# Performance work log

Measured on AMD Instinct MI355X. Metric: run time of the kernel, lower is better.

Reference implementation:

```python
import jax, jax.numpy as jnp
import numpy as np

LEAKY_SLOPE = 0.2  # LeakyReLU(0.2) attention activation from the torch module
HEADS = 4
RATES = (10, 25)


def _prod(v):
    r = 1
    for x in v:
        r *= x
    return r


def gat_conv(x_self, x_neigh, W, a_s, a_n):
    """Single GAT aggregation layer (aggregate_method='concat').
    x_self:  [..., F_in]
    x_neigh: [..., E, F_in] (leading dims reshape-compatible with x_self)
    W: [F_in, H*D], a_s/a_n: [H, D]
    Returns [..., H*D].
    """
    H = HEADS
    D = W.shape[1] // H
    lead = x_self.shape[:-1]
    E = x_neigh.shape[-2]
    z_s = (x_self @ W).reshape(lead + (H, D))                  # [..., H, D]
    z_n = (x_neigh @ W).reshape(lead + (E, H, D))              # [..., E, H, D]
    e_s = jnp.einsum('...hd,hd->...h', z_s, a_s)               # [..., H]
    e_n = jnp.einsum('...ehd,hd->...eh', z_n, a_n)             # [..., E, H]
    logits = jax.nn.leaky_relu(e_s[..., None, :] + e_n, LEAKY_SLOPE)
    alpha = jax.nn.softmax(logits, axis=-2)                    # softmax over neighbors E
    out = jnp.einsum('...eh,...ehd->...hd', alpha, z_n)        # attention-weighted sum
    return out.reshape(lead + (H * D,))


def setup_inputs() -> dict:
    key = jax.random.key(0)
    ks = jax.random.split(key, 10)
    B, F, HID, OUT = 1024, 128, 512, 256
    s = 0.05
    return {
        'h0': jax.random.normal(ks[0], (B, F), jnp.float32),
        'h1': jax.random.normal(ks[1], (B, RATES[0], F), jnp.float32),
        'h2': jax.random.normal(ks[2], (B, RATES[0] * RATES[1], F), jnp.float32),
        'W0': jax.random.normal(ks[3], (F, HID), jnp.float32) * s,
        'a0_s': jax.random.normal(ks[4], (HEADS, HID // HEADS), jnp.float32) * s,
        'a0_n': jax.random.normal(ks[5], (HEADS, HID // HEADS), jnp.float32) * s,
        'W1': jax.random.normal(ks[6], (HID, HID), jnp.float32) * s,
        'a1_s': jax.random.normal(ks[7], (HEADS, HID // HEADS), jnp.float32) * s,
        'a1_n': jax.random.normal(ks[8], (HEADS, HID // HEADS), jnp.float32) * s,
        'W_fc': jax.random.normal(ks[9], (HID, OUT), jnp.float32) * s,
    }


def reference(h0, h1, h2, W0, a0_s, a0_n, W1, a1_s, a1_n, W_fc):
    B = h0.shape[0]
    hs = [h0, h1, h2]
    layers = [(W0, a0_s, a0_n), (W1, a1_s, a1_n)]
    depth = len(RATES)
    # hierarchical sweep: layer i is applied to levels 0..depth-i-1
    for i, (W, a_s, a_n) in enumerate(layers):
        for j in range(depth - i):
            x_self = hs[j]
            x_neigh = hs[j + 1].reshape(B, _prod(RATES[:j]), RATES[j], -1)
            hs[j] = gat_conv(x_self, x_neigh, W, a_s, a_n)
    return hs[0] @ W_fc  # final Linear (no bias, no activation)
```

## Files before the change

### kernel.cpp

```cpp
#include <hip/hip_runtime.h>

__device__ __forceinline__ void gemm32(
    float* __restrict__ smem,
    const float* __restrict__ A, int lda,
    const float* __restrict__ B, int ldb,
    float* __restrict__ C, int ldc, int K,
    int m0, int col0) {
  float* As = smem;
  float* Bs = smem + 16 * 36;
  const int t = threadIdx.x;
  const int tn = t & 31, tm = t >> 5;
  const int lam = t >> 2, lak = (t & 3) * 4;
  const int lbk = t >> 4, lbn = (t & 15) * 8;
  float acc[4][4];
#pragma unroll
  for (int i = 0; i < 4; ++i)
#pragma unroll
    for (int j = 0; j < 4; ++j) acc[i][j] = 0.f;
  for (int k0 = 0; k0 < K; k0 += 16) {
    if (t < 128) {
      float4 av = *reinterpret_cast<const float4*>(A + (size_t)(m0 + lam) * lda + k0 + lak);
      As[(lak + 0) * 36 + lam] = av.x;
      As[(lak + 1) * 36 + lam] = av.y;
      As[(lak + 2) * 36 + lam] = av.z;
      As[(lak + 3) * 36 + lam] = av.w;
    }
    const float* bp = B + (size_t)(k0 + lbk) * ldb + col0 + lbn;
    float4 b0 = *reinterpret_cast<const float4*>(bp);
    float4 b1 = *reinterpret_cast<const float4*>(bp + 4);
    float* bd = &Bs[lbk * 132 + lbn];
    *reinterpret_cast<float4*>(bd) = b0;
    *reinterpret_cast<float4*>(bd + 4) = b1;
    __syncthreads();
#pragma unroll
    for (int kk = 0; kk < 16; ++kk) {
      float4 a4 = *reinterpret_cast<const float4*>(&As[kk * 36 + tm * 4]);
      float4 b4 = *reinterpret_cast<const float4*>(&Bs[kk * 132 + tn * 4]);
      float a[4] = {a4.x, a4.y, a4.z, a4.w};
      float b[4] = {b4.x, b4.y, b4.z, b4.w};
#pragma unroll
      for (int i = 0; i < 4; ++i)
#pragma unroll
        for (int j = 0; j < 4; ++j) acc[i][j] = fmaf(a[i], b[j], acc[i][j]);
    }
    __syncthreads();
  }
#pragma unroll
  for (int i = 0; i < 4; ++i) {
    float* cp = C + (size_t)(m0 + tm * 4 + i) * ldc + col0 + tn * 4;
    *reinterpret_cast<float4*>(cp) =
        make_float4(acc[i][0], acc[i][1], acc[i][2], acc[i][3]);
  }
}

template <int E>
__device__ __forceinline__ void gat128_item(
    float* __restrict__ smem,
    const float* __restrict__ xs, const float* __restrict__ xn,
    const float* __restrict__ waS, const float* __restrict__ waN,
    float* __restrict__ outp) {
  constexpr int MR = E + 1;
  constexpr int PASSES = (MR + 7) / 8;
  float* tile = smem;
  float* partial = smem + E * 128;
  const int t = threadIdx.x;
  const int el = t >> 5;
  const int f0 = (t & 31) * 4;
  float4 pre[PASSES];
#pragma unroll
  for (int p = 0; p < PASSES; ++p) {
    int e = p * 8 + el;
    if (e < E) pre[p] = *reinterpret_cast<const float4*>(xn + (size_t)e * 128 + f0);
    else if (e == E) pre[p] = *reinterpret_cast<const float4*>(xs + f0);
  }
  float4 wn[4], ws[4];
#pragma unroll
  for (int h = 0; h < 4; ++h) {
    wn[h] = *reinterpret_cast<const float4*>(waN + h * 128 + f0);
    ws[h] = *reinterpret_cast<const float4*>(waS + h * 128 + f0);
  }
#pragma unroll
  for (int p = 0; p < PASSES; ++p) {
    int e = p * 8 + el;
    if (e < MR) {
      float4 x = pre[p];
      if (e < E) *reinterpret_cast<float4*>(tile + e * 128 + f0) = x;
      float ph[4];
#pragma unroll
      for (int h = 0; h < 4; ++h) {
        float4 w = (e < E) ? wn[h] : ws[h];
        ph[h] = x.x * w.x + x.y * w.y + x.z * w.z + x.w * w.w;
      }
      const int b0 = t & 1, b1 = (t >> 1) & 1;
      float m0 = b0 ? ph[1] : ph[0];
      float o0 = b0 ? ph[0] : ph[1];
      float m1 = b0 ? ph[3] : ph[2];
      float o1 = b0 ? ph[2] : ph[3];
      m0 += __shfl_xor(o0, 1);
      m1 += __shfl_xor(o1, 1);
      float mk = b1 ? m1 : m0;
      float gv = b1 ? m0 : m1;
      mk += __shfl_xor(gv, 2);
      mk += __shfl_xor(mk, 4);
      mk += __shfl_xor(mk, 8);
      mk += __shfl_xor(mk, 16);
      if ((t & 31) < 4) partial[e * 4 + (t & 3)] = mk;
    }
  }
  __syncthreads();
  const int w = t >> 6, l = t & 63;
  float selfl = partial[E * 4 + w];
  float xv = -1e30f;
  if (l < E) {
    float x = selfl + partial[l * 4 + w];
    xv = (x > 0.f) ? x : 0.2f * x;
  }
  float m = xv;
  m = fmaxf(m, __shfl_xor(m, 1));
  m = fmaxf(m, __shfl_xor(m, 2));
  m = fmaxf(m, __shfl_xor(m, 4));
  m = fmaxf(m, __shfl_xor(m, 8));
  m = fmaxf(m, __shfl_xor(m, 16));
  m = fmaxf(m, __shfl_xor(m, 32));
  float pz = (l < E) ? __expf(xv - m) : 0.f;
  float s = pz;
  s += __shfl_xor(s, 1);
  s += __shfl_xor(s, 2);
  s += __shfl_xor(s, 4);
  s += __shfl_xor(s, 8);
  s += __shfl_xor(s, 16);
  s += __shfl_xor(s, 32);
  float alpha = pz * (1.f / s);
  float2 acc = make_float2(0.f, 0.f);
#pragma unroll
  for (int e = 0; e < E; ++e) {
    float a = __shfl(alpha, e);
    float2 x = *reinterpret_cast<const float2*>(tile + e * 128 + l * 2);
    acc.x = fmaf(a, x.x, acc.x);
    acc.y = fmaf(a, x.y, acc.y);
  }
  *reinterpret_cast<float2*>(outp + w * 128 + l * 2) = acc;
}

__device__ __forceinline__ void gat512_item(
    float* __restrict__ tile, float* __restrict__ partial,
    const float* __restrict__ xs, const float* __restrict__ xn,
    const float* __restrict__ vaS, const float* __restrict__ vaN,
    float* __restrict__ outp) {
  const int t = threadIdx.x;
  const int el = t >> 7, f0 = (t & 127) * 4;
  float4 vn[4], vs[4];
#pragma unroll
  for (int h = 0; h < 4; ++h) {
    vn[h] = *reinterpret_cast<const float4*>(vaN + h * 512 + f0);
    vs[h] = *reinterpret_cast<const float4*>(vaS + h * 512 + f0);
  }
#pragma unroll
  for (int p = 0; p < 6; ++p) {
    int e = p * 2 + el;
    if (e < 11) {
      const float* src = (e < 10) ? (xn + (size_t)e * 512 + f0) : (xs + f0);
      float4 x = *reinterpret_cast<const float4*>(src);
      if (e < 10) *reinterpret_cast<float4*>(tile + e * 512 + f0) = x;
      float ph[4];
#pragma unroll
      for (int h = 0; h < 4; ++h) {
        float4 w = (e < 10) ? vn[h] : vs[h];
        ph[h] = x.x * w.x + x.y * w.y + x.z * w.z + x.w * w.w;
      }
      const int b0 = t & 1, b1 = (t >> 1) & 1;
      float m0 = b0 ? ph[1] : ph[0];
      float o0 = b0 ? ph[0] : ph[1];
      float m1 = b0 ? ph[3] : ph[2];
      float o1 = b0 ? ph[2] : ph[3];
      m0 += __shfl_xor(o0, 1);
      m1 += __shfl_xor(o1, 1);
      float mk = b1 ? m1 : m0;
      float gv = b1 ? m0 : m1;
      mk += __shfl_xor(gv, 2);
      mk += __shfl_xor(mk, 4);
      mk += __shfl_xor(mk, 8);
      mk += __shfl_xor(mk, 16);
      mk += __shfl_xor(mk, 32);
      if ((t & 63) < 4) partial[e * 8 + ((t >> 6) & 1) * 4 + (t & 3)] = mk;
    }
  }
  __syncthreads();
  const int w = t >> 6, l = t & 63;
  float selfl = partial[10 * 8 + w] + partial[10 * 8 + 4 + w];
  float xv = -1e30f;
  if (l < 10) {
    float x = selfl + partial[l * 8 + w] + partial[l * 8 + 4 + w];
    xv = (x > 0.f) ? x : 0.2f * x;
  }
  float m = xv;
  m = fmaxf(m, __shfl_xor(m, 1));
  m = fmaxf(m, __shfl_xor(m, 2));
  m = fmaxf(m, __shfl_xor(m, 4));
  m = fmaxf(m, __shfl_xor(m, 8));
  m = fmaxf(m, __shfl_xor(m, 16));
  m = fmaxf(m, __shfl_xor(m, 32));
  float pz = (l < 10) ? __expf(xv - m) : 0.f;
  float s = pz;
  s += __shfl_xor(s, 1);
  s += __shfl_xor(s, 2);
  s += __shfl_xor(s, 4);
  s += __shfl_xor(s, 8);
  s += __shfl_xor(s, 16);
  s += __shfl_xor(s, 32);
  float alpha = pz * (1.f / s);
  float2 acc[4];
#pragma unroll
  for (int j = 0; j < 4; ++j) acc[j] = make_float2(0.f, 0.f);
#pragma unroll
  for (int e = 0; e < 10; ++e) {
    float a = __shfl(alpha, e);
#pragma unroll
    for (int j = 0; j < 4; ++j) {
      float2 x = *reinterpret_cast<const float2*>(tile + e * 512 + j * 128 + l * 2);
      acc[j].x = fmaf(a, x.x, acc[j].x);
      acc[j].y = fmaf(a, x.y, acc[j].y);
    }
  }
#pragma unroll
  for (int j = 0; j < 4; ++j)
    *reinterpret_cast<float2*>(outp + w * 512 + j * 128 + l * 2) = acc[j];
}

__global__ void __launch_bounds__(256) prepA(
    const float* __restrict__ W0, const float* __restrict__ a0s,
    const float* __restrict__ a0n,
    const float* __restrict__ W1, const float* __restrict__ a1s,
    const float* __restrict__ a1n, const float* __restrict__ Wfc,
    float* __restrict__ wa0s, float* __restrict__ wa0n,
    float* __restrict__ wa1s, float* __restrict__ wa1n,
    float* __restrict__ T) {
  __shared__ float smem[2688];
  const int b = blockIdx.x;
  if (b < 128) {
    int h = b >> 5, mb = (b >> 1) & 15, nb = b & 1;
    gemm32(smem, W1 + h * 128, 512, Wfc + (size_t)h * 32768, 256,
           T + (size_t)h * 131072, 256, 128, mb * 32, nb * 128);
    return;
  }
  int idx = (b - 128) * 256 + threadIdx.x;
  if (idx >= 5120) return;
  const float* W; const float* a; float* dst; int i; int FIN;
  if (idx < 512)       { W = W0; a = a0s; dst = wa0s; i = idx;        FIN = 128; }
  else if (idx < 1024) { W = W0; a = a0n; dst = wa0n; i = idx - 512;  FIN = 128; }
  else if (idx < 3072) { W = W1; a = a1s; dst = wa1s; i = idx - 1024; FIN = 512; }
  else                 { W = W1; a = a1n; dst = wa1n; i = idx - 3072; FIN = 512; }
  int f = i >> 2, h = i & 3;
  const float* wrow = W + (size_t)f * 512 + h * 128;
  const float* arow = a + h * 128;
  float v = 0.f;
#pragma unroll 8
  for (int d = 0; d < 128; ++d) v = fmaf(wrow[d], arow[d], v);
  dst[h * FIN + f] = v;
}

__global__ void __launch_bounds__(256) fusedB(
    const float* __restrict__ h0, const float* __restrict__ h1,
    const float* __restrict__ h2, const float* __restrict__ wa0s,
    const float* __restrict__ wa0n, float* __restrict__ xagg,
    const float* __restrict__ W0, const float* __restrict__ wa1s,
    const float* __restrict__ wa1n, const float* __restrict__ T,
    float* __restrict__ va1s, float* __restrict__ va1n,
    float* __restrict__ Wfinal) {
  __shared__ float smem[3304];
  const int b = blockIdx.x;
  if (b < 128) {
    int h = b >> 5, h0b = (b >> 3) & 3, mb = (b >> 1) & 3, nb = b & 1;
    gemm32(smem, W0 + h0b * 128, 512,
           T + (size_t)h * 131072 + (size_t)h0b * 32768, 256,
           Wfinal + (size_t)h * 131072 + (size_t)h0b * 32768, 256, 128,
           mb * 32, nb * 128);
    return;
  }
  if (b < 144) {
    int idx = (b - 128) * 256 + threadIdx.x;
    const float* wa = (idx < 2048) ? wa1s : wa1n;
    float* dst = (idx < 2048) ? va1s : va1n;
    int i = idx & 2047;
    int h = i >> 9, h0b = (i >> 7) & 3, f = i & 127;
    const float* w0row = W0 + (size_t)f * 512 + h0b * 128;
    const float* warow = wa + h * 512 + h0b * 128;
    float v = 0.f;
#pragma unroll 8
    for (int n = 0; n < 128; ++n) v = fmaf(w0row[n], warow[n], v);
    dst[i] = v;
    return;
  }
  if (b < 144 + 1024) {
    int n = b - 144;
    gat128_item<10>(smem, h0 + (size_t)n * 128, h1 + (size_t)n * 1280,
                    wa0s, wa0n, xagg + (size_t)n * 512);
    return;
  }
  int g = b - 1168;
  gat128_item<25>(smem, h1 + (size_t)g * 128, h2 + (size_t)g * 3200,
                  wa0s, wa0n, xagg + (size_t)(1024 + g) * 512);
}

__global__ void __launch_bounds__(256) gat_layer1(
    const float* __restrict__ xagg, const float* __restrict__ vaS,
    const float* __restrict__ vaN, float* __restrict__ aggx) {
  __shared__ float smem[5208];
  const int b = blockIdx.x;
  gat512_item(smem, smem + 5120, xagg + (size_t)b * 512,
              xagg + (size_t)(1024 + (size_t)b * 10) * 512, vaS, vaN,
              aggx + (size_t)b * 2048);
}

__global__ void __launch_bounds__(256) gemm_ksplit(
    const float* __restrict__ A, const float* __restrict__ B,
    float* __restrict__ Cpart) {
  __shared__ float smem[2688];
  const int ks = blockIdx.z;
  gemm32(smem, A + ks * 256, 2048, B + (size_t)ks * 65536, 256,
         Cpart + (size_t)ks * 262144, 256, 256, blockIdx.x * 32,
         blockIdx.y * 128);
}

__global__ void __launch_bounds__(256) reduce8(
    const float* __restrict__ Cpart, float* __restrict__ out) {
  int i = blockIdx.x * 256 + threadIdx.x;
  const float4* p = reinterpret_cast<const float4*>(Cpart) + i;
  float4 s = p[0];
#pragma unroll
  for (int ks = 1; ks < 8; ++ks) {
    float4 v = p[(size_t)ks * 65536];
    s.x += v.x; s.y += v.y; s.z += v.z; s.w += v.w;
  }
  reinterpret_cast<float4*>(out)[i] = s;
}

extern "C" void kernel_launch(void* const* d_in, const int* in_sizes, int n_in,
                              void* d_out, int out_size, void* d_ws, size_t ws_size,
                              hipStream_t stream) {
  const float* h0  = (const float*)d_in[0];
  const float* h1  = (const float*)d_in[1];
  const float* h2  = (const float*)d_in[2];
  const float* W0  = (const float*)d_in[3];
  const float* a0s = (const float*)d_in[4];
  const float* a0n = (const float*)d_in[5];
  const float* W1  = (const float*)d_in[6];
  const float* a1s = (const float*)d_in[7];
  const float* a1n = (const float*)d_in[8];
  const float* Wfc = (const float*)d_in[9];
  float* out = (float*)d_out;

  float* ws = (float*)d_ws;
  float* wa0s   = ws;
  float* wa0n   = wa0s + 512;
  float* wa1s   = wa0n + 512;
  float* wa1n   = wa1s + 2048;
  float* va1s   = wa1n + 2048;
  float* va1n   = va1s + 2048;
  float* T      = va1n + 2048;
  float* Wfinal = T + 524288;
  float* xaggA  = Wfinal + 524288;
  float* aggx   = xaggA + 11264 * 512;
  float* Cpart  = aggx + 2097152;

  prepA<<<148, 256, 0, stream>>>(W0, a0s, a0n, W1, a1s, a1n, Wfc,
                                 wa0s, wa0n, wa1s, wa1n, T);
  fusedB<<<11408, 256, 0, stream>>>(h0, h1, h2, wa0s, wa0n, xaggA,
                                    W0, wa1s, wa1n, T, va1s, va1n, Wfinal);
  gat_layer1<<<1024, 256, 0, stream>>>(xaggA, va1s, va1n, aggx);
  gemm_ksplit<<<dim3(32, 2, 8), 256, 0, stream>>>(aggx, Wfinal, Cpart);
  reduce8<<<256, 256, 0, stream>>>(Cpart, out);
}
```

Baseline: 256.1 us.

## Make fusedB a persistent grid that prefetches the next GAT item's loads

```diff
diff --git a/kernel.cpp b/kernel.cpp
--- a/kernel.cpp
+++ b/kernel.cpp
@@ -1,4 +1,6 @@
 #include <hip/hip_runtime.h>
+
+#define FB_GRID 2048
 
 __device__ __forceinline__ void gemm32(
     float* __restrict__ smem,
@@ -54,25 +56,14 @@
 }
 
 template <int E>
-__device__ __forceinline__ void gat128_item(
-    float* __restrict__ smem,
-    const float* __restrict__ xs, const float* __restrict__ xn,
-    const float* __restrict__ waS, const float* __restrict__ waN,
-    float* __restrict__ outp) {
+__device__ __forceinline__ void gat128_phase1(
+    float* __restrict__ tile, float* __restrict__ partial, const float4* pre,
+    const float* __restrict__ waS, const float* __restrict__ waN) {
   constexpr int MR = E + 1;
   constexpr int PASSES = (MR + 7) / 8;
-  float* tile = smem;
-  float* partial = smem + E * 128;
   const int t = threadIdx.x;
   const int el = t >> 5;
   const int f0 = (t & 31) * 4;
-  float4 pre[PASSES];
-#pragma unroll
-  for (int p = 0; p < PASSES; ++p) {
-    int e = p * 8 + el;
-    if (e < E) pre[p] = *reinterpret_cast<const float4*>(xn + (size_t)e * 128 + f0);
-    else if (e == E) pre[p] = *reinterpret_cast<const float4*>(xs + f0);
-  }
   float4 wn[4], ws[4];
 #pragma unroll
   for (int h = 0; h < 4; ++h) {
@@ -107,7 +98,13 @@
       if ((t & 31) < 4) partial[e * 4 + (t & 3)] = mk;
     }
   }
-  __syncthreads();
+}
+
+template <int E>
+__device__ __forceinline__ void gat128_phase23(
+    const float* __restrict__ tile, const float* __restrict__ partial,
+    float* __restrict__ outp) {
+  const int t = threadIdx.x;
   const int w = t >> 6, l = t & 63;
   float selfl = partial[E * 4 + w];
   float xv = -1e30f;
@@ -268,17 +265,17 @@
     float* __restrict__ va1s, float* __restrict__ va1n,
     float* __restrict__ Wfinal) {
   __shared__ float smem[3304];
-  const int b = blockIdx.x;
-  if (b < 128) {
-    int h = b >> 5, h0b = (b >> 3) & 3, mb = (b >> 1) & 3, nb = b & 1;
+  const int bid = blockIdx.x;
+  const int t = threadIdx.x;
+  if (bid < 128) {
+    int h = bid >> 5, h0b = (bid >> 3) & 3, mb = (bid >> 1) & 3, nb = bid & 1;
     gemm32(smem, W0 + h0b * 128, 512,
            T + (size_t)h * 131072 + (size_t)h0b * 32768, 256,
            Wfinal + (size_t)h * 131072 + (size_t)h0b * 32768, 256, 128,
            mb * 32, nb * 128);
-    return;
-  }
-  if (b < 144) {
-    int idx = (b - 128) * 256 + threadIdx.x;
+    __syncthreads();
+  } else if (bid < 144) {
+    int idx = (bid - 128) * 256 + t;
     const float* wa = (idx < 2048) ? wa1s : wa1n;
     float* dst = (idx < 2048) ? va1s : va1n;
     int i = idx & 2047;
@@ -289,17 +286,41 @@
 #pragma unroll 8
     for (int n = 0; n < 128; ++n) v = fmaf(w0row[n], warow[n], v);
     dst[i] = v;
-    return;
-  }
-  if (b < 144 + 1024) {
-    int n = b - 144;
-    gat128_item<10>(smem, h0 + (size_t)n * 128, h1 + (size_t)n * 1280,
-                    wa0s, wa0n, xagg + (size_t)n * 512);
-    return;
-  }
-  int g = b - 1168;
-  gat128_item<25>(smem, h1 + (size_t)g * 128, h2 + (size_t)g * 3200,
-                  wa0s, wa0n, xagg + (size_t)(1024 + g) * 512);
+  }
+
+  const int el = t >> 5, f0 = (t & 31) * 4;
+  auto loadPre = [&](int ai, float4* pr) {
+    const float* xs; const float* xn; int E;
+    if (ai < 10240) { xs = h1 + (size_t)ai * 128; xn = h2 + (size_t)ai * 3200; E = 25; }
+    else { int n = ai - 10240; xs = h0 + (size_t)n * 128; xn = h1 + (size_t)n * 1280; E = 10; }
+#pragma unroll
+    for (int p = 0; p < 4; ++p) {
+      int e = p * 8 + el;
+      if (e < E) pr[p] = *reinterpret_cast<const float4*>(xn + (size_t)e * 128 + f0);
+      else if (e == E) pr[p] = *reinterpret_cast<const float4*>(xs + f0);
+    }
+  };
+  float* tile = smem;
+  float* partial = smem + 3200;
+  float4 pre[4], pre2[4];
+  int a = (FB_GRID - 1) - bid;
+  loadPre(a, pre);
+  while (a < 11264) {
+    const bool e25 = (a < 10240);
+    if (e25) gat128_phase1<25>(tile, partial, pre, wa0s, wa0n);
+    else     gat128_phase1<10>(tile, partial, pre, wa0s, wa0n);
+    int nxt = a + FB_GRID;
+    if (nxt < 11264) loadPre(nxt, pre2);
+    __syncthreads();
+    float* outp = e25 ? xagg + (size_t)(1024 + a) * 512
+                      : xagg + (size_t)(a - 10240) * 512;
+    if (e25) gat128_phase23<25>(tile, partial, outp);
+    else     gat128_phase23<10>(tile, partial, outp);
+    __syncthreads();
+#pragma unroll
+    for (int p = 0; p < 4; ++p) pre[p] = pre2[p];
+    a = nxt;
+  }
 }
 
 __global__ void __launch_bounds__(256) gat_layer1(
@@ -365,8 +386,8 @@
 
   prepA<<<148, 256, 0, stream>>>(W0, a0s, a0n, W1, a1s, a1n, Wfc,
                                  wa0s, wa0n, wa1s, wa1n, T);
-  fusedB<<<11408, 256, 0, stream>>>(h0, h1, h2, wa0s, wa0n, xaggA,
-                                    W0, wa1s, wa1n, T, va1s, va1n, Wfinal);
+  fusedB<<<FB_GRID, 256, 0, stream>>>(h0, h1, h2, wa0s, wa0n, xaggA,
+                                      W0, wa1s, wa1n, T, va1s, va1n, Wfinal);
   gat_layer1<<<1024, 256, 0, stream>>>(xaggA, va1s, va1n, aggx);
   gemm_ksplit<<<dim3(32, 2, 8), 256, 0, stream>>>(aggx, Wfinal, Cpart);
   reduce8<<<256, 256, 0, stream>>>(Cpart, out);
```

New measurement: 279.3 us. 9.1% more time.
